# Kernel tuning notes

Hardware: AMD Instinct MI355X
Metric: run time of the kernel (lower is better)

Reference implementation:

```python
import jax, jax.numpy as jnp
from jax import lax
import numpy as np

D_MODEL = 512
H = 4
DK = 128
DV = 256
DFF = 2048
N_LAYERS = 12
N_LOC = 100  # 10x10 patches

CONV_SPECS = [(8, 3, 3), (16, 8, 3), (32, 16, 3), (32, 32, 3), (64, 32, 3),
              (64, 64, 3), (128, 64, 3), (128, 128, 3), (256, 128, 3), (512, 256, 2)]
RELU_AFTER = [False, True, False, True, True, True, True, True, True, False]


def setup_inputs() -> dict:
    key = jax.random.key(0)
    keys = iter(jax.random.split(key, 64))

    def nrm(shape, scale=0.02):
        return jax.random.normal(next(keys), shape, dtype=jnp.float32) * scale

    inp = {"x": jax.random.normal(next(keys), (1, 3, 200, 200), dtype=jnp.float32)}
    for i, (o, c, k) in enumerate(CONV_SPECS, 1):
        inp[f"cw{i}"] = nrm((o, c, k, k))
        inp[f"cb{i}"] = nrm((o,))
    inp["Wq"] = nrm((N_LAYERS, H, D_MODEL, DK))
    inp["Wk"] = nrm((N_LAYERS, H, D_MODEL, DK))
    inp["Wv"] = nrm((N_LAYERS, H, D_MODEL, DV))
    inp["Wo"] = nrm((N_LAYERS, H * DV, D_MODEL))
    inp["W1"] = nrm((N_LAYERS, D_MODEL, DFF))
    inp["b1"] = nrm((N_LAYERS, DFF))
    inp["W2"] = nrm((N_LAYERS, DFF, D_MODEL))
    inp["b2"] = nrm((N_LAYERS, D_MODEL))
    return inp


def _extract_patches(x):
    # x: [1,3,200,200] -> 100 patches of [3,20,20], index = i*10 + j
    # patch(i,j) = x[:, :, 20j:20(j+1), 20i:20(i+1)]  (i=cols outer, j=rows inner)
    x = x.reshape(3, 10, 20, 10, 20)            # [c, j_blk, row, i_blk, col]
    return jnp.transpose(x, (3, 1, 0, 2, 4)).reshape(N_LOC, 3, 20, 20)


def _local_embed(patches, cws, cbs):
    h = patches  # [100,3,20,20]
    for w, b, r in zip(cws, cbs, RELU_AFTER):
        h = lax.conv_general_dilated(h, w, (1, 1), 'VALID',
                                     dimension_numbers=('NCHW', 'OIHW', 'NCHW'))
        h = h + b[None, :, None, None]
        if r:
            h = jax.nn.relu(h)
    return h.reshape(N_LOC, D_MODEL)  # spatial reduced to 1x1


def _location_embeddings():
    # createLocationEmbedding(i, j) only uses i (the column-block coordinate).
    pos = jnp.repeat(jnp.arange(0, 200, 20, dtype=jnp.float32), 10)  # [100]
    k = jnp.arange(256, dtype=jnp.float32)
    inv = jnp.power(jnp.float32(10000.0), 2.0 * k / 256.0)
    ang = pos[:, None] / inv[None, :]  # [100,256]
    return jnp.concatenate([jnp.sin(ang), jnp.cos(ang)], axis=1)  # [100,512]


def _encoder_layer(h, Wq, Wk, Wv, Wo, W1, b1, W2, b2):
    # Multi-head attention; NOTE: scale uses K.size(0) = n_locations (faithful quirk).
    scale = 1.0 / jnp.sqrt(jnp.float32(N_LOC))
    q = jnp.einsum('nd,hdk->hnk', h, Wq)
    k = jnp.einsum('nd,hdk->hnk', h, Wk)
    v = jnp.einsum('nd,hdv->hnv', h, Wv)
    s = jnp.einsum('hnk,hmk->hnm', q, k) * scale
    a = jax.nn.softmax(s, axis=-1)
    o = jnp.einsum('hnm,hmv->hnv', a, v)
    o = jnp.transpose(o, (1, 0, 2)).reshape(N_LOC, H * DV)
    h = h + o @ Wo
    h = h + (jax.nn.relu(h @ W1 + b1) @ W2 + b2)
    return h


def reference(x, cw1, cb1, cw2, cb2, cw3, cb3, cw4, cb4, cw5, cb5,
              cw6, cb6, cw7, cb7, cw8, cb8, cw9, cb9, cw10, cb10,
              Wq, Wk, Wv, Wo, W1, b1, W2, b2):
    cws = [cw1, cw2, cw3, cw4, cw5, cw6, cw7, cw8, cw9, cw10]
    cbs = [cb1, cb2, cb3, cb4, cb5, cb6, cb7, cb8, cb9, cb10]
    patches = _extract_patches(x)
    h = _local_embed(patches, cws, cbs)
    h = h + _location_embeddings()
    for n in range(N_LAYERS):
        h = _encoder_layer(h, Wq[n], Wk[n], Wv[n], Wo[n], W1[n], b1[n], W2[n], b2[n])
    return h
```

## Files before the change

kernel.cpp:

```cpp
#include <hip/hip_runtime.h>
#include <math.h>

#define NLOC 100

typedef __attribute__((ext_vector_type(8))) _Float16 half8;
typedef __attribute__((ext_vector_type(4))) float f32x4;

#define H_OFF     0
#define QKV_OFF   51200
#define OCAT_OFF  256000
#define FFN_OFF   307200
#define ACTA_OFF  409600
#define ACTB_OFF  729664
#define CWH_OFF   1049728
#define CW1_OFF   1605504
#define WQKVT_OFF 1605824
#define WOT_OFF   7897280
#define W1T_OFF   11043008
#define W2T_OFF   17334464

struct WPack { const float* w[9]; };
struct WTArgs { const float* src[6]; };

__global__ __launch_bounds__(256) void cw1repack(const float* __restrict__ w, float* __restrict__ w4)
{
    int idx = blockIdx.x*256 + threadIdx.x;
    if (idx >= 288) return;
    int c = idx & 3;
    int r = idx >> 2;
    int oc = r / 9, kk = r - oc*9;
    int ky = kk/3, kx = kk - ky*3;
    float v = 0.f;
    if (c < 3) v = w[((oc*3 + c)*3 + ky)*3 + kx];
    w4[idx] = v;
}

__global__ __launch_bounds__(256) void cwrepack(WPack wp, unsigned short* __restrict__ dst)
{
    const int Cin[9]  = {8,16,32,32,64,64,128,128,256};
    const int shift[9]= {3,4,5,5,6,6,7,7,8};
    const int KS[9]   = {3,3,3,3,3,3,3,3,2};
    const int Kpad[9] = {96,160,288,288,576,576,1152,1152,1024};
    const int off[10] = {0,1536,6656,15872,34304,71168,144896,292352,587264,1111552};
    const int total = 1111552;
    for (int i = blockIdx.x*blockDim.x + threadIdx.x; i < total; i += gridDim.x*blockDim.x) {
        int l = 0;
        while (i >= off[l+1]) ++l;
        int rem = i - off[l];
        int kp = Kpad[l];
        int oc = rem / kp;
        int k  = rem - oc*kp;
        int ci = Cin[l];
        int ic = k & (ci - 1);
        int kk = k >> shift[l];
        int ks = KS[l], k2 = ks*ks;
        float v = 0.f;
        if (kk < k2) {
            int ky = kk / ks, kx = kk - ky*ks;
            v = wp.w[l][((oc*ci + ic)*ks + ky)*ks + kx];
        }
        _Float16 hv = (_Float16)v;
        dst[i] = __builtin_bit_cast(unsigned short, hv);
    }
}

__global__ __launch_bounds__(256) void wtrans_all(WTArgs wa,
    unsigned short* __restrict__ wqkvt, unsigned short* __restrict__ w1t,
    unsigned short* __restrict__ w2t, unsigned short* __restrict__ wot)
{
    const int pre[7]  = {0, 3072, 6144, 12288, 24576, 36864, 43008};
    const int tX[6]   = {4, 4, 8, 64, 16, 16};
    const int Kd[6]   = {512, 512, 512, 512, 2048, 1024};
    const int Nd[6]   = {128, 128, 256, 2048, 512, 512};
    const int mpl[6]  = {4, 4, 4, 1, 1, 1};
    const int dls[6]  = {1048576, 1048576, 1048576, 1048576, 1048576, 524288};
    const int dbase[6]= {0, 262144, 524288, 0, 0, 0};
    __shared__ float tsh[32][33];
    int b = blockIdx.x;
    int seg = 0;
    while (b >= pre[seg+1]) ++seg;
    int lb = b - pre[seg];
    int K = Kd[seg], N = Nd[seg];
    int tpm = (N/32)*(K/32);
    int mz = lb / tpm;
    int r = lb - mz*tpm;
    int ty_ = r / tX[seg];
    int tx_ = r - ty_*tX[seg];
    int layer = mz / mpl[seg];
    int mi = mz - layer*mpl[seg];
    const float* s = wa.src[seg] + (size_t)mz * K * N;
    unsigned short* base = (seg < 3) ? wqkvt : (seg == 3 ? w1t : (seg == 4 ? w2t : wot));
    unsigned short* d = base + (size_t)layer*dls[seg] + dbase[seg] + (size_t)mi * N * K;
    int n0 = tx_*32, k0 = ty_*32;
    int lx = threadIdx.x & 31, ly = threadIdx.x >> 5;
    #pragma unroll
    for (int i = 0; i < 32; i += 8) tsh[ly + i][lx] = s[(size_t)(k0 + ly + i)*N + n0 + lx];
    __syncthreads();
    #pragma unroll
    for (int i = 0; i < 32; i += 8) {
        _Float16 hv = (_Float16)tsh[lx][ly + i];
        d[(size_t)(n0 + ly + i)*K + k0 + lx] = __builtin_bit_cast(unsigned short, hv);
    }
}

__global__ __launch_bounds__(256) void conv1k(const float* __restrict__ x,
    const float4* __restrict__ w4, const float* __restrict__ bias, unsigned short* __restrict__ out)
{
    int idx = blockIdx.x*256 + threadIdx.x;
    if (idx >= 32400) return;
    int p = idx / 324;
    int s = idx - p*324;
    int sy = s / 18, sx = s - sy*18;
    int pi = p/10, pj = p - pi*10;
    const float* xb = x + (pj*20 + sy)*200 + pi*20 + sx;
    float acc[8];
    #pragma unroll
    for (int o = 0; o < 8; ++o) acc[o] = bias[o];
    #pragma unroll
    for (int ky = 0; ky < 3; ++ky)
        #pragma unroll
        for (int kx = 0; kx < 3; ++kx) {
            float r = xb[ky*200 + kx];
            float g = xb[40000 + ky*200 + kx];
            float bch = xb[80000 + ky*200 + kx];
            #pragma unroll
            for (int o = 0; o < 8; ++o) {
                float4 wv = w4[o*9 + ky*3 + kx];
                acc[o] += r*wv.x + g*wv.y + bch*wv.z;
            }
        }
    unsigned short h8[8];
    #pragma unroll
    for (int o = 0; o < 8; ++o) {
        _Float16 hv = (_Float16)acc[o];
        h8[o] = __builtin_bit_cast(unsigned short, hv);
    }
    *(uint4*)(out + (size_t)idx*8) = *(const uint4*)h8;
}

template<int CIN, int COUT, int KS, int HIN, int WIN, int HOUT, int WOUT, int KPAD, int RELU, int LAST>
__global__ __launch_bounds__(256) void convM(const unsigned short* __restrict__ in,
    const unsigned short* __restrict__ wth, const float* __restrict__ bias,
    unsigned short* __restrict__ out, float* __restrict__ hout)
{
    constexpr int HW = HOUT*WOUT;
    constexpr int M = 100*HW;
    constexpr int MT = (M + 15)/16;
    constexpr int NT = COUT/16;
    int wave = threadIdx.x >> 6, lane = threadIdx.x & 63;
    int t = blockIdx.x*4 + wave;
    if (t >= MT*NT) return;
    int mt = t % MT, nt = t / MT;
    int mrow = lane & 15, quad = lane >> 4;
    int mg = mt*16 + mrow; if (mg >= M) mg = M - 1;
    int p = mg / HW, s = mg - p*HW;
    int sy = s / WOUT, sx = s - sy*WOUT;
    const unsigned short* ap = in + ((size_t)((p*HIN + sy)*WIN + sx))*CIN;
    const unsigned short* bp = wth + ((size_t)(nt*16 + mrow))*KPAD + quad*8;
    f32x4 acc = {0.f, 0.f, 0.f, 0.f};
    #pragma unroll
    for (int k0 = 0; k0 < KPAD; k0 += 32) {
        int k = k0 + quad*8;
        int kk = k / CIN; if (kk > KS*KS - 1) kk = KS*KS - 1;
        int ky = kk / KS, kx = kk - ky*KS;
        uint4 av = *(const uint4*)(ap + (ky*WIN + kx)*CIN + (k & (CIN-1)));
        uint4 bv = *(const uint4*)(bp + k0);
        acc = __builtin_amdgcn_mfma_f32_16x16x32_f16(
            __builtin_bit_cast(half8, av), __builtin_bit_cast(half8, bv), acc, 0, 0, 0);
    }
    int n = nt*16 + mrow;
    float bv = bias[n];
    #pragma unroll
    for (int r = 0; r < 4; ++r) {
        int m = mt*16 + quad*4 + r;
        if (m < M) {
            float v = acc[r] + bv;
            if (RELU) v = fmaxf(v, 0.f);
            if (LAST) {
                int pi = m / 10;
                float pos = 20.f * (float)pi;
                int dd = n & 255;
                float inv = powf(10000.f, (float)dd * (1.f/128.f));
                float ang = pos / inv;
                v += (n < 256) ? sinf(ang) : cosf(ang);
                hout[(size_t)m*512 + n] = v;
            } else {
                _Float16 hv = (_Float16)v;
                out[(size_t)m*COUT + n] = __builtin_bit_cast(unsigned short, hv);
            }
        }
    }
}

template<int KCHUNK, int ABITS, int RELU, int ATOMIC, int STOREH>
__global__ __launch_bounds__(256) void gemm16(
    const void* __restrict__ Av, int lda,
    const unsigned short* __restrict__ Bt, int K,
    const float* __restrict__ bias,
    float* __restrict__ C, unsigned short* __restrict__ Ch, int ldc)
{
    int lane = threadIdx.x & 63;
    int wave = threadIdx.x >> 6;
    int mrow = lane & 15, quad = lane >> 4;
    int n0 = blockIdx.x*64 + wave*16;
    int m0 = blockIdx.y*16;
    int arow = m0 + mrow; if (arow > 99) arow = 99;
    int k0 = blockIdx.z * KCHUNK;
    const unsigned short* bp = Bt + (size_t)(n0 + mrow)*K + quad*8 + k0;
    f32x4 acc = {0.f, 0.f, 0.f, 0.f};
    if (ABITS == 16) {
        const unsigned short* ap = (const unsigned short*)Av + (size_t)arow*lda + quad*8 + k0;
        #pragma unroll 8
        for (int k = 0; k < KCHUNK; k += 32) {
            uint4 au = *(const uint4*)(ap + k);
            uint4 bu = *(const uint4*)(bp + k);
            acc = __builtin_amdgcn_mfma_f32_16x16x32_f16(
                __builtin_bit_cast(half8, au), __builtin_bit_cast(half8, bu), acc, 0, 0, 0);
        }
    } else {
        const float* ap = (const float*)Av + (size_t)arow*lda + quad*8 + k0;
        #pragma unroll 8
        for (int k = 0; k < KCHUNK; k += 32) {
            float4 f0 = *(const float4*)(ap + k);
            float4 f1 = *(const float4*)(ap + k + 4);
            half8 af;
            af[0] = (_Float16)f0.x; af[1] = (_Float16)f0.y;
            af[2] = (_Float16)f0.z; af[3] = (_Float16)f0.w;
            af[4] = (_Float16)f1.x; af[5] = (_Float16)f1.y;
            af[6] = (_Float16)f1.z; af[7] = (_Float16)f1.w;
            uint4 bu = *(const uint4*)(bp + k);
            acc = __builtin_amdgcn_mfma_f32_16x16x32_f16(
                af, __builtin_bit_cast(half8, bu), acc, 0, 0, 0);
        }
    }
    int n = n0 + mrow;
    float bv = (bias != nullptr && blockIdx.z == 0) ? bias[n] : 0.f;
    #pragma unroll
    for (int r = 0; r < 4; ++r) {
        int row = m0 + quad*4 + r;
        if (row < 100) {
            float v = acc[r] + bv;
            if (RELU) v = fmaxf(v, 0.f);
            if (ATOMIC) atomicAdd(&C[(size_t)row*ldc + n], v);
            else if (C != nullptr) C[(size_t)row*ldc + n] = v;
            if (STOREH) {
                _Float16 hv = (_Float16)v;
                Ch[(size_t)row*ldc + n] = __builtin_bit_cast(unsigned short, hv);
            }
        }
    }
}

__global__ __launch_bounds__(256) void attn_kernel(
    const float* __restrict__ qkv, unsigned short* __restrict__ ocat)
{
    __shared__ float qr[128];
    __shared__ float p[100];
    __shared__ float red[2];
    int bx = blockIdx.x;
    int hh = bx / 100, nn = bx - hh*100;
    int t = threadIdx.x;
    if (t < 128) qr[t] = qkv[(size_t)nn*2048 + hh*128 + t];
    __syncthreads();
    float sv = 0.f;
    if (t < 100) {
        const float4* kp = (const float4*)(qkv + (size_t)t*2048 + 512 + hh*128);
        const float4* q4 = (const float4*)qr;
        float s0=0.f, s1=0.f, s2=0.f, s3=0.f;
        #pragma unroll 8
        for (int j = 0; j < 32; ++j) {
            float4 a = q4[j], b = kp[j];
            s0 += a.x*b.x; s1 += a.y*b.y; s2 += a.z*b.z; s3 += a.w*b.w;
        }
        sv = (s0+s1+s2+s3) * 0.1f;
        p[t] = sv;
    }
    __syncthreads();
    if (t < 64) {
        float m = fmaxf(p[t], (t+64 < 100) ? p[t+64] : -1e30f);
        for (int o = 32; o > 0; o >>= 1) m = fmaxf(m, __shfl_down(m, o));
        if (t == 0) red[0] = m;
    }
    __syncthreads();
    float mx = red[0];
    if (t < 100) p[t] = expf(sv - mx);
    __syncthreads();
    if (t < 64) {
        float s = p[t] + ((t+64 < 100) ? p[t+64] : 0.f);
        for (int o = 32; o > 0; o >>= 1) s += __shfl_down(s, o);
        if (t == 0) red[1] = s;
    }
    __syncthreads();
    float inv = 1.0f / red[1];
    const float* vp = qkv + 1024 + hh*256 + t;
    float acc = 0.f;
    #pragma unroll 4
    for (int m = 0; m < 100; ++m) acc += p[m] * vp[(size_t)m*2048];
    _Float16 hv = (_Float16)(acc * inv);
    ocat[(size_t)nn*1024 + hh*256 + t] = __builtin_bit_cast(unsigned short, hv);
}

__global__ __launch_bounds__(256) void copyk(const float* __restrict__ s, float* __restrict__ d, int n)
{
    int i = blockIdx.x*256 + threadIdx.x;
    if (i < n) d[i] = s[i];
}

extern "C" void kernel_launch(void* const* d_in, const int* in_sizes, int n_in,
                              void* d_out, int out_size, void* d_ws, size_t ws_size,
                              hipStream_t stream)
{
    const float* x = (const float*)d_in[0];
    const float* cw1 = (const float*)d_in[1];
    const float* cb[10];
    WPack wpk;
    for (int i = 0; i < 10; ++i) cb[i] = (const float*)d_in[2 + 2*i];
    for (int i = 0; i < 9; ++i)  wpk.w[i] = (const float*)d_in[3 + 2*i];
    const float* Wq = (const float*)d_in[21];
    const float* Wk = (const float*)d_in[22];
    const float* Wv = (const float*)d_in[23];
    const float* Wo = (const float*)d_in[24];
    const float* W1 = (const float*)d_in[25];
    const float* b1 = (const float*)d_in[26];
    const float* W2 = (const float*)d_in[27];
    const float* b2 = (const float*)d_in[28];

    float* ws = (float*)d_ws;
    float* h   = ws + H_OFF;
    float* qkv = ws + QKV_OFF;
    unsigned short* ocat = (unsigned short*)(ws + OCAT_OFF);
    unsigned short* ffn  = (unsigned short*)(ws + FFN_OFF);
    unsigned short* aA   = (unsigned short*)(ws + ACTA_OFF);
    unsigned short* aB   = (unsigned short*)(ws + ACTB_OFF);
    unsigned short* cwh  = (unsigned short*)(ws + CWH_OFF);
    float* cw14 = ws + CW1_OFF;
    unsigned short* wqkvt = (unsigned short*)(ws + WQKVT_OFF);
    unsigned short* wot   = (unsigned short*)(ws + WOT_OFF);
    unsigned short* w1t   = (unsigned short*)(ws + W1T_OFF);
    unsigned short* w2t   = (unsigned short*)(ws + W2T_OFF);

    cw1repack<<<2, 256, 0, stream>>>(cw1, cw14);
    cwrepack<<<2172, 256, 0, stream>>>(wpk, cwh);
    WTArgs wargs;
    wargs.src[0] = Wq; wargs.src[1] = Wk; wargs.src[2] = Wv;
    wargs.src[3] = W1; wargs.src[4] = W2; wargs.src[5] = Wo;
    wtrans_all<<<43008, 256, 0, stream>>>(wargs, wqkvt, w1t, w2t, wot);

    conv1k<<<127, 256, 0, stream>>>(x, (const float4*)cw14, cb[0], aA);
    convM<8,  16, 3,18,18,16,16,  96,1,0><<<400, 256, 0, stream>>>(aA, cwh + 0,      cb[1], aB, nullptr);
    convM<16, 32, 3,16,16,14,14, 160,0,0><<<613, 256, 0, stream>>>(aB, cwh + 1536,   cb[2], aA, nullptr);
    convM<32, 32, 3,14,14,12,12, 288,1,0><<<450, 256, 0, stream>>>(aA, cwh + 6656,   cb[3], aB, nullptr);
    convM<32, 64, 3,12,12,10,10, 288,1,0><<<625, 256, 0, stream>>>(aB, cwh + 15872,  cb[4], aA, nullptr);
    convM<64, 64, 3,10,10, 8, 8, 576,1,0><<<400, 256, 0, stream>>>(aA, cwh + 34304,  cb[5], aB, nullptr);
    convM<64,128, 3, 8, 8, 6, 6, 576,1,0><<<450, 256, 0, stream>>>(aB, cwh + 71168,  cb[6], aA, nullptr);
    convM<128,128,3, 6, 6, 4, 4,1152,1,0><<<200, 256, 0, stream>>>(aA, cwh + 144896, cb[7], aB, nullptr);
    convM<128,256,3, 4, 4, 2, 2,1152,1,0><<<100, 256, 0, stream>>>(aB, cwh + 292352, cb[8], aA, nullptr);
    convM<256,512,2, 2, 2, 1, 1,1024,0,1><<<56,  256, 0, stream>>>(aA, cwh + 587264, cb[9], nullptr, h);

    for (int n = 0; n < 12; ++n) {
        const unsigned short* Bq  = wqkvt + (size_t)n * 2048 * 512;
        const unsigned short* Bo  = wot   + (size_t)n * 512 * 1024;
        const unsigned short* Bf1 = w1t   + (size_t)n * 2048 * 512;
        const unsigned short* Bf2 = w2t   + (size_t)n * 512 * 2048;
        gemm16<512,32,0,0,0><<<dim3(32, 7, 1), 256, 0, stream>>>(h, 512, Bq, 512,
            nullptr, qkv, nullptr, 2048);
        attn_kernel<<<400, 256, 0, stream>>>(qkv, ocat);
        gemm16<256,16,0,1,0><<<dim3(8, 7, 4), 256, 0, stream>>>(ocat, 1024, Bo, 1024,
            nullptr, h, nullptr, 512);
        gemm16<512,32,1,0,1><<<dim3(32, 7, 1), 256, 0, stream>>>(h, 512, Bf1, 512,
            b1 + (size_t)n*2048, nullptr, ffn, 2048);
        gemm16<512,16,0,1,0><<<dim3(8, 7, 4), 256, 0, stream>>>(ffn, 2048, Bf2, 2048,
            b2 + (size_t)n*512, h, nullptr, 512);
    }
    copyk<<<200, 256, 0, stream>>>(h, (float*)d_out, NLOC*512);
}
```

Measured before the change: 914.4 us.

## Fuse transformer layers into one persistent cooperative kernel with grid syncs

Replaces the 61 per-layer kernel launches (four GEMMs, attention, and the final copy) with a single cooperative kernel of 256 blocks. Stages are separated by grid.sync() and each wave takes a fixed GEMM tile, which is meant to remove launch gaps and tail effects between the many small kernels. The weight-transpose kernel is also changed to handle 64x32 tiles and write packed 32-bit fp16 pairs, halving its block count. The risk is that grid-wide barriers cost more than the launches they replace, and each stage now runs with fewer concurrent blocks.

```diff
diff --git a/kernel.cpp b/kernel.cpp
--- a/kernel.cpp
+++ b/kernel.cpp
@@ -1,5 +1,8 @@
 #include <hip/hip_runtime.h>
+#include <hip/hip_cooperative_groups.h>
 #include <math.h>
+
+namespace cg = cooperative_groups;
 
 #define NLOC 100
 
@@ -21,6 +24,20 @@
 
 struct WPack { const float* w[9]; };
 struct WTArgs { const float* src[6]; };
+
+struct TParams {
+    const unsigned short* wqkvt;
+    const unsigned short* wot;
+    const unsigned short* w1t;
+    const unsigned short* w2t;
+    const float* b1;
+    const float* b2;
+    float* h;
+    float* qkv;
+    unsigned short* ocat;
+    unsigned short* ffn;
+    float* out;
+};
 
 __global__ __launch_bounds__(256) void cw1repack(const float* __restrict__ w, float* __restrict__ w4)
 {
@@ -68,38 +85,47 @@
     unsigned short* __restrict__ wqkvt, unsigned short* __restrict__ w1t,
     unsigned short* __restrict__ w2t, unsigned short* __restrict__ wot)
 {
-    const int pre[7]  = {0, 3072, 6144, 12288, 24576, 36864, 43008};
-    const int tX[6]   = {4, 4, 8, 64, 16, 16};
+    const int pre[7]  = {0, 1536, 3072, 6144, 12288, 18432, 21504};
+    const int tXd[6]  = {4, 4, 8, 64, 16, 16};
     const int Kd[6]   = {512, 512, 512, 512, 2048, 1024};
     const int Nd[6]   = {128, 128, 256, 2048, 512, 512};
     const int mpl[6]  = {4, 4, 4, 1, 1, 1};
     const int dls[6]  = {1048576, 1048576, 1048576, 1048576, 1048576, 524288};
     const int dbase[6]= {0, 262144, 524288, 0, 0, 0};
-    __shared__ float tsh[32][33];
+    __shared__ float tsh[64][33];
     int b = blockIdx.x;
     int seg = 0;
     while (b >= pre[seg+1]) ++seg;
     int lb = b - pre[seg];
     int K = Kd[seg], N = Nd[seg];
-    int tpm = (N/32)*(K/32);
+    int tX = tXd[seg];
+    int tpm = tX * (K >> 6);
     int mz = lb / tpm;
     int r = lb - mz*tpm;
-    int ty_ = r / tX[seg];
-    int tx_ = r - ty_*tX[seg];
+    int ty_ = r / tX;
+    int tx_ = r - ty_*tX;
     int layer = mz / mpl[seg];
     int mi = mz - layer*mpl[seg];
     const float* s = wa.src[seg] + (size_t)mz * K * N;
     unsigned short* base = (seg < 3) ? wqkvt : (seg == 3 ? w1t : (seg == 4 ? w2t : wot));
     unsigned short* d = base + (size_t)layer*dls[seg] + dbase[seg] + (size_t)mi * N * K;
-    int n0 = tx_*32, k0 = ty_*32;
+    int n0 = tx_*32, k0 = ty_*64;
     int lx = threadIdx.x & 31, ly = threadIdx.x >> 5;
     #pragma unroll
-    for (int i = 0; i < 32; i += 8) tsh[ly + i][lx] = s[(size_t)(k0 + ly + i)*N + n0 + lx];
+    for (int i = 0; i < 8; ++i) {
+        int k = i*8 + ly;
+        tsh[k][lx] = s[(size_t)(k0 + k)*N + n0 + lx];
+    }
     __syncthreads();
     #pragma unroll
-    for (int i = 0; i < 32; i += 8) {
-        _Float16 hv = (_Float16)tsh[lx][ly + i];
-        d[(size_t)(n0 + ly + i)*K + k0 + lx] = __builtin_bit_cast(unsigned short, hv);
+    for (int i = 0; i < 4; ++i) {
+        int nn = i*8 + ly;
+        _Float16 h0 = (_Float16)tsh[2*lx][nn];
+        _Float16 h1 = (_Float16)tsh[2*lx+1][nn];
+        unsigned int wd = (unsigned int)__builtin_bit_cast(unsigned short, h0)
+                        | ((unsigned int)__builtin_bit_cast(unsigned short, h1) << 16);
+        unsigned int* du = (unsigned int*)(d + (size_t)(n0 + nn)*K + k0);
+        du[lx] = wd;
     }
 }
 
@@ -192,118 +218,181 @@
     }
 }
 
-template<int KCHUNK, int ABITS, int RELU, int ATOMIC, int STOREH>
-__global__ __launch_bounds__(256) void gemm16(
-    const void* __restrict__ Av, int lda,
-    const unsigned short* __restrict__ Bt, int K,
-    const float* __restrict__ bias,
-    float* __restrict__ C, unsigned short* __restrict__ Ch, int ldc)
-{
-    int lane = threadIdx.x & 63;
-    int wave = threadIdx.x >> 6;
+__global__ __launch_bounds__(256) void transformer_all(TParams P)
+{
+    cg::grid_group grid = cg::this_grid();
+    __shared__ float qr[128];
+    __shared__ float pbuf[100];
+    __shared__ float red[2];
+
+    int t = threadIdx.x;
+    int wave = t >> 6, lane = t & 63;
+    int gw = blockIdx.x*4 + wave;
     int mrow = lane & 15, quad = lane >> 4;
-    int n0 = blockIdx.x*64 + wave*16;
-    int m0 = blockIdx.y*16;
-    int arow = m0 + mrow; if (arow > 99) arow = 99;
-    int k0 = blockIdx.z * KCHUNK;
-    const unsigned short* bp = Bt + (size_t)(n0 + mrow)*K + quad*8 + k0;
-    f32x4 acc = {0.f, 0.f, 0.f, 0.f};
-    if (ABITS == 16) {
-        const unsigned short* ap = (const unsigned short*)Av + (size_t)arow*lda + quad*8 + k0;
-        #pragma unroll 8
-        for (int k = 0; k < KCHUNK; k += 32) {
-            uint4 au = *(const uint4*)(ap + k);
-            uint4 bu = *(const uint4*)(bp + k);
-            acc = __builtin_amdgcn_mfma_f32_16x16x32_f16(
-                __builtin_bit_cast(half8, au), __builtin_bit_cast(half8, bu), acc, 0, 0, 0);
-        }
-    } else {
-        const float* ap = (const float*)Av + (size_t)arow*lda + quad*8 + k0;
-        #pragma unroll 8
-        for (int k = 0; k < KCHUNK; k += 32) {
-            float4 f0 = *(const float4*)(ap + k);
-            float4 f1 = *(const float4*)(ap + k + 4);
-            half8 af;
-            af[0] = (_Float16)f0.x; af[1] = (_Float16)f0.y;
-            af[2] = (_Float16)f0.z; af[3] = (_Float16)f0.w;
-            af[4] = (_Float16)f1.x; af[5] = (_Float16)f1.y;
-            af[6] = (_Float16)f1.z; af[7] = (_Float16)f1.w;
-            uint4 bu = *(const uint4*)(bp + k);
-            acc = __builtin_amdgcn_mfma_f32_16x16x32_f16(
-                af, __builtin_bit_cast(half8, bu), acc, 0, 0, 0);
-        }
-    }
-    int n = n0 + mrow;
-    float bv = (bias != nullptr && blockIdx.z == 0) ? bias[n] : 0.f;
-    #pragma unroll
-    for (int r = 0; r < 4; ++r) {
-        int row = m0 + quad*4 + r;
-        if (row < 100) {
-            float v = acc[r] + bv;
-            if (RELU) v = fmaxf(v, 0.f);
-            if (ATOMIC) atomicAdd(&C[(size_t)row*ldc + n], v);
-            else if (C != nullptr) C[(size_t)row*ldc + n] = v;
-            if (STOREH) {
-                _Float16 hv = (_Float16)v;
-                Ch[(size_t)row*ldc + n] = __builtin_bit_cast(unsigned short, hv);
-            }
-        }
-    }
-}
-
-__global__ __launch_bounds__(256) void attn_kernel(
-    const float* __restrict__ qkv, unsigned short* __restrict__ ocat)
-{
-    __shared__ float qr[128];
-    __shared__ float p[100];
-    __shared__ float red[2];
-    int bx = blockIdx.x;
-    int hh = bx / 100, nn = bx - hh*100;
-    int t = threadIdx.x;
-    if (t < 128) qr[t] = qkv[(size_t)nn*2048 + hh*128 + t];
-    __syncthreads();
-    float sv = 0.f;
-    if (t < 100) {
-        const float4* kp = (const float4*)(qkv + (size_t)t*2048 + 512 + hh*128);
-        const float4* q4 = (const float4*)qr;
-        float s0=0.f, s1=0.f, s2=0.f, s3=0.f;
-        #pragma unroll 8
-        for (int j = 0; j < 32; ++j) {
-            float4 a = q4[j], b = kp[j];
-            s0 += a.x*b.x; s1 += a.y*b.y; s2 += a.z*b.z; s3 += a.w*b.w;
-        }
-        sv = (s0+s1+s2+s3) * 0.1f;
-        p[t] = sv;
-    }
-    __syncthreads();
-    if (t < 64) {
-        float m = fmaxf(p[t], (t+64 < 100) ? p[t+64] : -1e30f);
-        for (int o = 32; o > 0; o >>= 1) m = fmaxf(m, __shfl_down(m, o));
-        if (t == 0) red[0] = m;
-    }
-    __syncthreads();
-    float mx = red[0];
-    if (t < 100) p[t] = expf(sv - mx);
-    __syncthreads();
-    if (t < 64) {
-        float s = p[t] + ((t+64 < 100) ? p[t+64] : 0.f);
-        for (int o = 32; o > 0; o >>= 1) s += __shfl_down(s, o);
-        if (t == 0) red[1] = s;
-    }
-    __syncthreads();
-    float inv = 1.0f / red[1];
-    const float* vp = qkv + 1024 + hh*256 + t;
-    float acc = 0.f;
-    #pragma unroll 4
-    for (int m = 0; m < 100; ++m) acc += p[m] * vp[(size_t)m*2048];
-    _Float16 hv = (_Float16)(acc * inv);
-    ocat[(size_t)nn*1024 + hh*256 + t] = __builtin_bit_cast(unsigned short, hv);
-}
-
-__global__ __launch_bounds__(256) void copyk(const float* __restrict__ s, float* __restrict__ d, int n)
-{
-    int i = blockIdx.x*256 + threadIdx.x;
-    if (i < n) d[i] = s[i];
+
+    for (int n = 0; n < 12; ++n) {
+        const unsigned short* Bq  = P.wqkvt + (size_t)n * 2048 * 512;
+        const unsigned short* Bo  = P.wot   + (size_t)n * 512 * 1024;
+        const unsigned short* Bf1 = P.w1t   + (size_t)n * 2048 * 512;
+        const unsigned short* Bf2 = P.w2t   + (size_t)n * 512 * 2048;
+        const float* b1l = P.b1 + (size_t)n * 2048;
+        const float* b2l = P.b2 + (size_t)n * 512;
+
+        if (gw < 896) {
+            int nt = gw & 127, mt = gw >> 7;
+            int n0 = nt*16, m0 = mt*16;
+            int arow = m0 + mrow; if (arow > 99) arow = 99;
+            const float* ap = P.h + (size_t)arow*512 + quad*8;
+            const unsigned short* bp = Bq + (size_t)(n0 + mrow)*512 + quad*8;
+            f32x4 acc = {0.f,0.f,0.f,0.f};
+            #pragma unroll 8
+            for (int k = 0; k < 512; k += 32) {
+                float4 f0 = *(const float4*)(ap + k);
+                float4 f1 = *(const float4*)(ap + k + 4);
+                half8 af;
+                af[0]=(_Float16)f0.x; af[1]=(_Float16)f0.y; af[2]=(_Float16)f0.z; af[3]=(_Float16)f0.w;
+                af[4]=(_Float16)f1.x; af[5]=(_Float16)f1.y; af[6]=(_Float16)f1.z; af[7]=(_Float16)f1.w;
+                uint4 bu = *(const uint4*)(bp + k);
+                acc = __builtin_amdgcn_mfma_f32_16x16x32_f16(
+                    af, __builtin_bit_cast(half8, bu), acc, 0, 0, 0);
+            }
+            int nn = n0 + mrow;
+            #pragma unroll
+            for (int r = 0; r < 4; ++r) {
+                int row = m0 + quad*4 + r;
+                if (row < 100) P.qkv[(size_t)row*2048 + nn] = acc[r];
+            }
+        }
+        grid.sync();
+
+        for (int item = blockIdx.x; item < 400; item += 256) {
+            int hh = item / 100, nq = item - hh*100;
+            if (t < 128) qr[t] = P.qkv[(size_t)nq*2048 + hh*128 + t];
+            __syncthreads();
+            float sv = 0.f;
+            if (t < 100) {
+                const float4* kp = (const float4*)(P.qkv + (size_t)t*2048 + 512 + hh*128);
+                const float4* q4 = (const float4*)qr;
+                float s0=0.f, s1=0.f, s2=0.f, s3=0.f;
+                #pragma unroll 8
+                for (int j = 0; j < 32; ++j) {
+                    float4 a = q4[j], b = kp[j];
+                    s0 += a.x*b.x; s1 += a.y*b.y; s2 += a.z*b.z; s3 += a.w*b.w;
+                }
+                sv = (s0+s1+s2+s3) * 0.1f;
+                pbuf[t] = sv;
+            }
+            __syncthreads();
+            if (t < 64) {
+                float m = fmaxf(pbuf[t], (t+64 < 100) ? pbuf[t+64] : -1e30f);
+                for (int o = 32; o > 0; o >>= 1) m = fmaxf(m, __shfl_down(m, o));
+                if (t == 0) red[0] = m;
+            }
+            __syncthreads();
+            float mx = red[0];
+            if (t < 100) pbuf[t] = expf(sv - mx);
+            __syncthreads();
+            if (t < 64) {
+                float s = pbuf[t] + ((t+64 < 100) ? pbuf[t+64] : 0.f);
+                for (int o = 32; o > 0; o >>= 1) s += __shfl_down(s, o);
+                if (t == 0) red[1] = s;
+            }
+            __syncthreads();
+            float inv = 1.0f / red[1];
+            const float* vp = P.qkv + 1024 + hh*256 + t;
+            float acc = 0.f;
+            #pragma unroll 4
+            for (int m = 0; m < 100; ++m) acc += pbuf[m] * vp[(size_t)m*2048];
+            _Float16 hv = (_Float16)(acc * inv);
+            P.ocat[(size_t)nq*1024 + hh*256 + t] = __builtin_bit_cast(unsigned short, hv);
+            __syncthreads();
+        }
+        grid.sync();
+
+        if (gw < 896) {
+            int kz = gw / 224;
+            int rr = gw - kz*224;
+            int nt = rr & 31, mt = rr >> 5;
+            int n0 = nt*16, m0 = mt*16, k0 = kz*256;
+            int arow = m0 + mrow; if (arow > 99) arow = 99;
+            const unsigned short* ap = P.ocat + (size_t)arow*1024 + quad*8 + k0;
+            const unsigned short* bp = Bo + (size_t)(n0 + mrow)*1024 + quad*8 + k0;
+            f32x4 acc = {0.f,0.f,0.f,0.f};
+            #pragma unroll
+            for (int k = 0; k < 256; k += 32) {
+                uint4 au = *(const uint4*)(ap + k);
+                uint4 bu = *(const uint4*)(bp + k);
+                acc = __builtin_amdgcn_mfma_f32_16x16x32_f16(
+                    __builtin_bit_cast(half8, au), __builtin_bit_cast(half8, bu), acc, 0, 0, 0);
+            }
+            int nn = n0 + mrow;
+            #pragma unroll
+            for (int r2 = 0; r2 < 4; ++r2) {
+                int row = m0 + quad*4 + r2;
+                if (row < 100) atomicAdd(&P.h[(size_t)row*512 + nn], acc[r2]);
+            }
+        }
+        grid.sync();
+
+        if (gw < 896) {
+            int nt = gw & 127, mt = gw >> 7;
+            int n0 = nt*16, m0 = mt*16;
+            int arow = m0 + mrow; if (arow > 99) arow = 99;
+            const float* ap = P.h + (size_t)arow*512 + quad*8;
+            const unsigned short* bp = Bf1 + (size_t)(n0 + mrow)*512 + quad*8;
+            f32x4 acc = {0.f,0.f,0.f,0.f};
+            #pragma unroll 8
+            for (int k = 0; k < 512; k += 32) {
+                float4 f0 = *(const float4*)(ap + k);
+                float4 f1 = *(const float4*)(ap + k + 4);
+                half8 af;
+                af[0]=(_Float16)f0.x; af[1]=(_Float16)f0.y; af[2]=(_Float16)f0.z; af[3]=(_Float16)f0.w;
+                af[4]=(_Float16)f1.x; af[5]=(_Float16)f1.y; af[6]=(_Float16)f1.z; af[7]=(_Float16)f1.w;
+                uint4 bu = *(const uint4*)(bp + k);
+                acc = __builtin_amdgcn_mfma_f32_16x16x32_f16(
+                    af, __builtin_bit_cast(half8, bu), acc, 0, 0, 0);
+            }
+            int nn = n0 + mrow;
+            float bv = b1l[nn];
+            #pragma unroll
+            for (int r = 0; r < 4; ++r) {
+                int row = m0 + quad*4 + r;
+                if (row < 100) {
+                    float v = fmaxf(acc[r] + bv, 0.f);
+                    _Float16 hv = (_Float16)v;
+                    P.ffn[(size_t)row*2048 + nn] = __builtin_bit_cast(unsigned short, hv);
+                }
+            }
+        }
+        grid.sync();
+
+        if (gw < 896) {
+            int kz = gw / 224;
+            int rr = gw - kz*224;
+            int nt = rr & 31, mt = rr >> 5;
+            int n0 = nt*16, m0 = mt*16, k0 = kz*512;
+            int arow = m0 + mrow; if (arow > 99) arow = 99;
+            const unsigned short* ap = P.ffn + (size_t)arow*2048 + quad*8 + k0;
+            const unsigned short* bp = Bf2 + (size_t)(n0 + mrow)*2048 + quad*8 + k0;
+            f32x4 acc = {0.f,0.f,0.f,0.f};
+            #pragma unroll 8
+            for (int k = 0; k < 512; k += 32) {
+                uint4 au = *(const uint4*)(ap + k);
+                uint4 bu = *(const uint4*)(bp + k);
+                acc = __builtin_amdgcn_mfma_f32_16x16x32_f16(
+                    __builtin_bit_cast(half8, au), __builtin_bit_cast(half8, bu), acc, 0, 0, 0);
+            }
+            int nn = n0 + mrow;
+            float bv = (kz == 0) ? b2l[nn] : 0.f;
+            #pragma unroll
+            for (int r2 = 0; r2 < 4; ++r2) {
+                int row = m0 + quad*4 + r2;
+                if (row < 100) atomicAdd(&P.h[(size_t)row*512 + nn], acc[r2] + bv);
+            }
+        }
+        grid.sync();
+    }
+    for (int i = blockIdx.x*256 + t; i < 51200; i += 65536) P.out[i] = P.h[i];
 }
 
 extern "C" void kernel_launch(void* const* d_in, const int* in_sizes, int n_in,
@@ -344,7 +433,7 @@
     WTArgs wargs;
     wargs.src[0] = Wq; wargs.src[1] = Wk; wargs.src[2] = Wv;
     wargs.src[3] = W1; wargs.src[4] = W2; wargs.src[5] = Wo;
-    wtrans_all<<<43008, 256, 0, stream>>>(wargs, wqkvt, w1t, w2t, wot);
+    wtrans_all<<<21504, 256, 0, stream>>>(wargs, wqkvt, w1t, w2t, wot);
 
     conv1k<<<127, 256, 0, stream>>>(x, (const float4*)cw14, cb[0], aA);
     convM<8,  16, 3,18,18,16,16,  96,1,0><<<400, 256, 0, stream>>>(aA, cwh + 0,      cb[1], aB, nullptr);
@@ -357,20 +446,12 @@
     convM<128,256,3, 4, 4, 2, 2,1152,1,0><<<100, 256, 0, stream>>>(aB, cwh + 292352, cb[8], aA, nullptr);
     convM<256,512,2, 2, 2, 1, 1,1024,0,1><<<56,  256, 0, stream>>>(aA, cwh + 587264, cb[9], nullptr, h);
 
-    for (int n = 0; n < 12; ++n) {
-        const unsigned short* Bq  = wqkvt + (size_t)n * 2048 * 512;
-        const unsigned short* Bo  = wot   + (size_t)n * 512 * 1024;
-        const unsigned short* Bf1 = w1t   + (size_t)n * 2048 * 512;
-        const unsigned short* Bf2 = w2t   + (size_t)n * 512 * 2048;
-        gemm16<512,32,0,0,0><<<dim3(32, 7, 1), 256, 0, stream>>>(h, 512, Bq, 512,
-            nullptr, qkv, nullptr, 2048);
-        attn_kernel<<<400, 256, 0, stream>>>(qkv, ocat);
-        gemm16<256,16,0,1,0><<<dim3(8, 7, 4), 256, 0, stream>>>(ocat, 1024, Bo, 1024,
-            nullptr, h, nullptr, 512);
-        gemm16<512,32,1,0,1><<<dim3(32, 7, 1), 256, 0, stream>>>(h, 512, Bf1, 512,
-            b1 + (size_t)n*2048, nullptr, ffn, 2048);
-        gemm16<512,16,0,1,0><<<dim3(8, 7, 4), 256, 0, stream>>>(ffn, 2048, Bf2, 2048,
-            b2 + (size_t)n*512, h, nullptr, 512);
-    }
-    copyk<<<200, 256, 0, stream>>>(h, (float*)d_out, NLOC*512);
-}
+    TParams P;
+    P.wqkvt = wqkvt; P.wot = wot; P.w1t = w1t; P.w2t = w2t;
+    P.b1 = b1; P.b2 = b2;
+    P.h = h; P.qkv = qkv; P.ocat = ocat; P.ffn = ffn;
+    P.out = (float*)d_out;
+    void* kargs[] = { &P };
+    hipLaunchCooperativeKernel((const void*)transformer_all, dim3(256), dim3(256),
+                               kargs, 0, stream);
+}
```

Result: slower. 2.628 ms (+187.4%).
